# Kernel tuning notes

Hardware: AMD Instinct MI355X
Metric: run time of the kernel (lower is better)

Reference implementation:

```python
import jax, jax.numpy as jnp
import numpy as np

BITS = 4
MASK = (1 << BITS) - 1  # 15


def _dequant(qweight, scales, qzeros, groupsize):
    # qweight: [in//32*bits, out] int32; 8 nibbles packed per int32 along rows.
    out_f = qweight.shape[1]
    shifts = jnp.arange(0, 32, BITS, dtype=jnp.int32)  # [8]
    # [rows, 8, out] -> unpacked int weights in [0, 15]
    w = (qweight[:, None, :] >> shifts[None, :, None]) & MASK
    w = w.reshape(-1, groupsize, out_f)  # [n_groups, groupsize, out]
    s = scales.reshape(-1, 1, out_f)     # [n_groups, 1, out]
    z = qzeros.reshape(-1, 1, out_f)
    W = s * w.astype(scales.dtype) - z * s
    return W.reshape(-1, out_f)          # [in, out]


def setup_inputs() -> dict:
    key = jax.random.key(0)
    k1, k2, k3, k4, k5 = jax.random.split(key, 5)
    B, S, IN, OUT, G = 4, 2048, 4096, 4096, 64
    x = jax.random.normal(k1, (B, S, IN), dtype=jnp.float16)
    qweight = jax.random.randint(k2, (IN // 32 * BITS, OUT), 0, 2147483647, dtype=jnp.int32)
    scales = (jax.random.uniform(k3, (IN // G, OUT), dtype=jnp.float32) * 0.01 + 0.001).astype(jnp.float16)
    qzeros = (jax.random.uniform(k4, (IN // G, OUT), dtype=jnp.float32) * 15.0).astype(jnp.float16)
    bias = jax.random.normal(k5, (OUT,), dtype=jnp.float16)
    return {"x": x, "qweight": qweight, "scales": scales, "qzeros": qzeros,
            "bias": bias, "groupsize": G, "bits": BITS}


def reference(x, qweight, scales, qzeros, bias, groupsize, bits):
    W = _dequant(qweight, scales, qzeros, groupsize)  # [in, out] fp16
    return jnp.matmul(x, W) + bias
```

## Files before the change

kernel.cpp:

```cpp
#include <hip/hip_runtime.h>
#include <stdint.h>
#include <stddef.h>

typedef __bf16 bf16;
typedef __bf16 bf16x8 __attribute__((ext_vector_type(8)));
typedef float  f32x4  __attribute__((ext_vector_type(4)));

#define GLOBAL_AS(p) ((const __attribute__((address_space(1))) void*)(p))
#define LDS_AS(p)    ((__attribute__((address_space(3))) void*)(p))

__device__ __forceinline__ void gload_lds16(const bf16* g, bf16* l) {
    __builtin_amdgcn_global_load_lds(GLOBAL_AS(g), LDS_AS(l), 16, 0, 0);
}

__global__ __launch_bounds__(256)
void convert_x_kernel(const float* __restrict__ x, bf16* __restrict__ xb, long n8) {
    long t = (long)blockIdx.x * blockDim.x + threadIdx.x;
    if (t >= n8) return;
    const f32x4* p = (const f32x4*)(x + t * 8);
    f32x4 a = p[0], b = p[1];
    bf16x8 v;
#pragma unroll
    for (int j = 0; j < 4; ++j) { v[j] = (bf16)a[j]; v[4 + j] = (bf16)b[j]; }
    *(bf16x8*)(xb + t * 8) = v;
}

__global__ __launch_bounds__(256)
void dequant_wt64_kernel(const uint32_t* __restrict__ qw,
                         const float* __restrict__ scales,
                         const float* __restrict__ qzeros,
                         bf16* __restrict__ Wt,
                         int N, int K, int rows_per_group) {
    const int i = blockIdx.x * 256 + threadIdx.x;
    const int w = i >> 6, l = i & 63;
    const int nr8 = K >> 6;
    const int r8 = w % nr8;
    const int o  = (w / nr8) * 8 + (l >> 3);
    const int rr = l & 7;
    const int r  = r8 * 8 + rr;
    if (o >= N) return;
    const uint32_t q = qw[(size_t)r * N + o];
    const int g = r / rows_per_group;
    const float s = scales[(size_t)g * N + o];
    const float z = qzeros[(size_t)g * N + o];
    const float nsz = -s * z;
    bf16x8 v;
#pragma unroll
    for (int j = 0; j < 8; ++j)
        v[j] = (bf16)fmaf((float)((q >> (4 * j)) & 15u), s, nsz);
    *(bf16x8*)(Wt + ((size_t)r8 * N + o) * 64 + rr * 8) = v;
}

constexpr int BM2 = 256, BN2 = 256, BK2 = 64;

#define SB()    __builtin_amdgcn_sched_barrier(0)
#define BAR()   __builtin_amdgcn_s_barrier()
#define LGKM0() asm volatile("s_waitcnt lgkmcnt(0)" ::: "memory")
#define VMCNT(N) asm volatile("s_waitcnt vmcnt(" #N ")" ::: "memory")

#define PHASE_TAIL(A, B, IBASE)                          \
    SB();                                                \
    __builtin_amdgcn_s_setprio(1);                       \
    MFMA_HALF(A, B, IBASE);                              \
    __builtin_amdgcn_s_setprio(0);                       \
    SB();                                                \
    LGKM0();                                             \
    BAR();                                               \
    SB()

#define MFMA_HALF(A, B, IBASE)                                             \
    _Pragma("unroll")                                                      \
    for (int i_ = 0; i_ < 4; ++i_) {                                       \
        _Pragma("unroll")                                                  \
        for (int j_ = 0; j_ < 4; ++j_)                                     \
            acc[(IBASE) + i_][j_] = __builtin_amdgcn_mfma_f32_16x16x32_bf16( \
                (A)[(IBASE) + i_], (B)[j_], acc[(IBASE) + i_][j_], 0, 0, 0); \
    }

#define READ_A4(DST, BUF, KH, LO)                                          \
    _Pragma("unroll")                                                      \
    for (int i_ = (LO); i_ < (LO) + 4; ++i_)                               \
        DST[i_] = *(const bf16x8*)(&As[BUF][(wm * 128 + i_ * 16 + lrow) * 64 \
                                           + (((lhi + 4 * (KH)) ^ swz) * 8)]);
#define READ_B4(DST, BUF, KH)                                              \
    _Pragma("unroll")                                                      \
    for (int j_ = 0; j_ < 4; ++j_)                                         \
        DST[j_] = *(const bf16x8*)(&Bs[BUF][(wn * 64 + j_ * 16 + lrow) * 64 \
                                           + (((lhi + 4 * (KH)) ^ swz) * 8)]);

__global__ __launch_bounds__(512, 2)
void gemm8_kernel(const bf16* __restrict__ Ab,
                  const bf16* __restrict__ Bt,
                  const float* __restrict__ bias,
                  float* __restrict__ out,
                  int M, int N, int K, int nbx) {
    __shared__ __align__(16) bf16 As[2][BM2 * BK2];
    __shared__ __align__(16) bf16 Bs[2][BN2 * BK2];

    const int tid  = threadIdx.x;
    const int lane = tid & 63;
    const int wave = tid >> 6;
    const int wm = wave >> 2;
    const int wn = wave & 3;

    const int nwg = gridDim.x;
    int wg = blockIdx.x;
    {
        const int q = nwg >> 3, r = nwg & 7;
        const int xcd = wg & 7, off = wg >> 3;
        wg = (xcd < r ? xcd * (q + 1) : r * (q + 1) + (xcd - r) * q) + off;
    }
    const int nby = nwg / nbx;
    const int bx = wg / nby;
    const int by = wg % nby;
    const int m0 = by * BM2;
    const int n0 = bx * BN2;

    const int lrow = lane & 15;
    const int lhi  = lane >> 4;
    const int swz  = (lrow >> 1) & 7;

    const int NT = K >> 6;
    const int NI = NT >> 1;

    auto stageA = [&](int tIdx, int half, int buf) {
#pragma unroll
        for (int it = 0; it < 2; ++it) {
            const int q  = tid + it * 512;
            const int rl = q >> 3;
            const int cl = (q & 7) ^ ((rl >> 1) & 7);
            gload_lds16(Ab + (size_t)(m0 + half * 128 + rl) * K + tIdx * 64 + cl * 8,
                        &As[buf][half * 8192 + q * 8]);
        }
    };
    auto stageB = [&](int tIdx, int half, int buf) {
#pragma unroll
        for (int it = 0; it < 2; ++it) {
            const int q  = tid + it * 512;
            const int rl = q >> 3;
            const int cl = (q & 7) ^ ((rl >> 1) & 7);
            gload_lds16(Bt + ((size_t)tIdx * N + n0 + half * 128 + rl) * 64 + cl * 8,
                        &Bs[buf][half * 8192 + q * 8]);
        }
    };

    f32x4 acc[8][4];
#pragma unroll
    for (int i = 0; i < 8; ++i)
#pragma unroll
        for (int j = 0; j < 4; ++j) acc[i][j] = (f32x4){0.f, 0.f, 0.f, 0.f};

    stageA(0, 0, 0); stageA(0, 1, 0); stageB(0, 0, 0); stageB(0, 1, 0);
    stageA(1, 0, 1); stageA(1, 1, 1);
    VMCNT(4);
    BAR();
    SB();

    bf16x8 fa0[8], fa1[8], fb0[4], fb1[4];
    READ_A4(fa0, 0, 0, 0);
    READ_B4(fb0, 0, 0);
    LGKM0();
    SB();

    for (int i2 = 0; i2 < NI; ++i2) {
        const int t0  = 2 * i2;
        const int tB1 = t0 + 1;
        const int tS2 = (t0 + 2 < NT) ? t0 + 2 : NT - 1;
        const int tS3 = (t0 + 3 < NT) ? t0 + 3 : NT - 1;

        READ_A4(fa0, 0, 0, 4);
        stageB(tB1, 0, 1);
        stageB(tB1, 1, 1);
        PHASE_TAIL(fa0, fb0, 0);

        READ_A4(fa1, 0, 1, 0);
        READ_B4(fb1, 0, 1);
        PHASE_TAIL(fa0, fb0, 4);

        READ_A4(fa1, 0, 1, 4);
        stageB(tS2, 0, 0);
        stageB(tS2, 1, 0);
        PHASE_TAIL(fa1, fb1, 0);

        stageA(tS2, 0, 0);
        VMCNT(6);
        BAR();
        SB();
        READ_A4(fa0, 1, 0, 0);
        READ_B4(fb0, 1, 0);
        PHASE_TAIL(fa1, fb1, 4);

        READ_A4(fa0, 1, 0, 4);
        stageA(tS2, 1, 0);
        PHASE_TAIL(fa0, fb0, 0);

        READ_A4(fa1, 1, 1, 0);
        READ_B4(fb1, 1, 1);
        PHASE_TAIL(fa0, fb0, 4);

        READ_A4(fa1, 1, 1, 4);
        PHASE_TAIL(fa1, fb1, 0);

        stageA(tS3, 0, 1);
        stageA(tS3, 1, 1);
        VMCNT(4);
        BAR();
        SB();
        READ_A4(fa0, 0, 0, 0);
        READ_B4(fb0, 0, 0);
        PHASE_TAIL(fa1, fb1, 4);
    }

    asm volatile("s_waitcnt vmcnt(0)" ::: "memory");

#pragma unroll
    for (int j = 0; j < 4; ++j) {
        const int col = n0 + wn * 64 + j * 16 + lrow;
        const float bv = bias[col];
#pragma unroll
        for (int i = 0; i < 8; ++i) {
            const int rbase = m0 + wm * 128 + i * 16 + lhi * 4;
#pragma unroll
            for (int r = 0; r < 4; ++r)
                out[(size_t)(rbase + r) * N + col] = acc[i][j][r] + bv;
        }
    }
}

constexpr int BM = 128, BN = 128, BK = 32;

__global__ __launch_bounds__(256)
void gemm_fused_kernel(const float* __restrict__ Af,
                       const uint32_t* __restrict__ qw,
                       const float* __restrict__ scales,
                       const float* __restrict__ qzeros,
                       const float* __restrict__ bias,
                       float* __restrict__ out,
                       int M, int N, int K, int G) {
    __shared__ __align__(16) bf16 As2[BM * BK];
    __shared__ __align__(16) bf16 Bs2[BN * BK];

    const int tid  = threadIdx.x;
    const int lane = tid & 63;
    const int wave = tid >> 6;
    const int wmm = wave & 1;
    const int wnn = wave >> 1;
    const int m0 = blockIdx.y * BM;
    const int n0 = blockIdx.x * BN;

    const int lr = lane & 15;
    const int lk8 = (lane >> 4) * 8;

    f32x4 acc[4][4];
#pragma unroll
    for (int i = 0; i < 4; ++i)
#pragma unroll
        for (int j = 0; j < 4; ++j) acc[i][j] = (f32x4){0.f, 0.f, 0.f, 0.f};

    for (int kt = 0; kt < K; kt += BK) {
#pragma unroll
        for (int it = 0; it < 2; ++it) {
            const int c = tid + it * 256;
            const int row = c >> 2;
            const int kc  = (c & 3) * 8;
            const f32x4* p = (const f32x4*)(Af + (size_t)(m0 + row) * K + kt + kc);
            f32x4 a = p[0], b = p[1];
            bf16x8 v;
#pragma unroll
            for (int j = 0; j < 4; ++j) { v[j] = (bf16)a[j]; v[4 + j] = (bf16)b[j]; }
            *(bf16x8*)(As2 + row * BK + kc) = v;
        }
        const int g = kt / G;
#pragma unroll
        for (int it = 0; it < 2; ++it) {
            const int idx = tid + it * 256;
            const int rl = idx >> 7;
            const int nl = idx & 127;
            uint32_t q = qw[(size_t)(kt / 8 + rl) * N + n0 + nl];
            float s = scales[(size_t)g * N + n0 + nl];
            float z = qzeros[(size_t)g * N + n0 + nl];
            float nsz = -s * z;
            bf16x8 v;
#pragma unroll
            for (int j = 0; j < 8; ++j)
                v[j] = (bf16)fmaf((float)((q >> (4 * j)) & 15u), s, nsz);
            *(bf16x8*)(Bs2 + nl * BK + rl * 8) = v;
        }
        __syncthreads();

        bf16x8 a[4], b[4];
#pragma unroll
        for (int i = 0; i < 4; ++i)
            a[i] = *(const bf16x8*)(As2 + (wmm * 64 + i * 16 + lr) * BK + lk8);
#pragma unroll
        for (int j = 0; j < 4; ++j)
            b[j] = *(const bf16x8*)(Bs2 + (wnn * 64 + j * 16 + lr) * BK + lk8);

#pragma unroll
        for (int i = 0; i < 4; ++i)
#pragma unroll
            for (int j = 0; j < 4; ++j)
                acc[i][j] = __builtin_amdgcn_mfma_f32_16x16x32_bf16(
                    a[i], b[j], acc[i][j], 0, 0, 0);
        __syncthreads();
    }

#pragma unroll
    for (int j = 0; j < 4; ++j) {
        const int col = n0 + wnn * 64 + j * 16 + (lane & 15);
        const float bv = bias[col];
#pragma unroll
        for (int i = 0; i < 4; ++i) {
            const int rbase = m0 + wmm * 64 + i * 16 + (lane >> 4) * 4;
#pragma unroll
            for (int r = 0; r < 4; ++r)
                out[(size_t)(rbase + r) * N + col] = acc[i][j][r] + bv;
        }
    }
}

extern "C" void kernel_launch(void* const* d_in, const int* in_sizes, int n_in,
                              void* d_out, int out_size, void* d_ws, size_t ws_size,
                              hipStream_t stream) {
    const float*    x      = (const float*)d_in[0];
    const uint32_t* qw     = (const uint32_t*)d_in[1];
    const float*    scales = (const float*)d_in[2];
    const float*    qzeros = (const float*)d_in[3];
    const float*    bias   = (const float*)d_in[4];
    float*          out    = (float*)d_out;

    const int N = in_sizes[4];
    const int K = (in_sizes[1] / N) * 8;
    const int M = in_sizes[0] / K;
    const int G = K / (in_sizes[2] / N);

    const size_t xb_bytes = (size_t)M * K * sizeof(bf16);
    const size_t wt_bytes = (size_t)N * K * sizeof(bf16);

    const bool shape_ok = (M % BM2 == 0) && (N % BN2 == 0) && (K % 128 == 0) &&
                          (G % 8 == 0);

    if (shape_ok && ws_size >= xb_bytes + wt_bytes) {
        bf16* Xb = (bf16*)d_ws;
        bf16* Wt = (bf16*)((char*)d_ws + xb_bytes);
        const long n8 = (long)M * K / 8;
        convert_x_kernel<<<(int)((n8 + 255) / 256), 256, 0, stream>>>(x, Xb, n8);
        const long dq_threads = ((long)K >> 6) * (N / 8) * 64;
        dequant_wt64_kernel<<<(int)((dq_threads + 255) / 256), 256, 0, stream>>>(
            qw, scales, qzeros, Wt, N, K, G / 8);
        const int nbx = N / BN2;
        const int nwg = nbx * (M / BM2);
        gemm8_kernel<<<nwg, 512, 0, stream>>>(Xb, Wt, bias, out, M, N, K, nbx);
    } else {
        dim3 grid(N / BN, M / BM);
        gemm_fused_kernel<<<grid, 256, 0, stream>>>(
            x, qw, scales, qzeros, bias, out, M, N, K, G);
    }
}
```

Measured before the change: 500.0 us.

## Reschedule GEMM main loop with precomputed load pointers and merged barrier phases

After: 518.2 us. +3.6%, slower.

```diff
diff --git a/kernel.cpp b/kernel.cpp
--- a/kernel.cpp
+++ b/kernel.cpp
@@ -58,16 +58,6 @@
 #define LGKM0() asm volatile("s_waitcnt lgkmcnt(0)" ::: "memory")
 #define VMCNT(N) asm volatile("s_waitcnt vmcnt(" #N ")" ::: "memory")
 
-#define PHASE_TAIL(A, B, IBASE)                          \
-    SB();                                                \
-    __builtin_amdgcn_s_setprio(1);                       \
-    MFMA_HALF(A, B, IBASE);                              \
-    __builtin_amdgcn_s_setprio(0);                       \
-    SB();                                                \
-    LGKM0();                                             \
-    BAR();                                               \
-    SB()
-
 #define MFMA_HALF(A, B, IBASE)                                             \
     _Pragma("unroll")                                                      \
     for (int i_ = 0; i_ < 4; ++i_) {                                       \
@@ -76,6 +66,25 @@
             acc[(IBASE) + i_][j_] = __builtin_amdgcn_mfma_f32_16x16x32_bf16( \
                 (A)[(IBASE) + i_], (B)[j_], acc[(IBASE) + i_][j_], 0, 0, 0); \
     }
+
+#define PHASE_TAIL(A, B, IBASE)                          \
+    SB();                                                \
+    __builtin_amdgcn_s_setprio(1);                       \
+    MFMA_HALF(A, B, IBASE);                              \
+    __builtin_amdgcn_s_setprio(0);                       \
+    LGKM0();                                             \
+    BAR();                                               \
+    SB()
+
+#define PHASE_TAIL_VM4(A, B, IBASE)                      \
+    SB();                                                \
+    __builtin_amdgcn_s_setprio(1);                       \
+    MFMA_HALF(A, B, IBASE);                              \
+    __builtin_amdgcn_s_setprio(0);                       \
+    LGKM0();                                             \
+    VMCNT(4);                                            \
+    BAR();                                               \
+    SB()
 
 #define READ_A4(DST, BUF, KH, LO)                                          \
     _Pragma("unroll")                                                      \
@@ -123,25 +132,40 @@
     const int NT = K >> 6;
     const int NI = NT >> 1;
 
-    auto stageA = [&](int tIdx, int half, int buf) {
+    const bf16* aSrc[2][2];
+    const bf16* bSrc[2][2];
+#pragma unroll
+    for (int h = 0; h < 2; ++h)
 #pragma unroll
         for (int it = 0; it < 2; ++it) {
             const int q  = tid + it * 512;
             const int rl = q >> 3;
             const int cl = (q & 7) ^ ((rl >> 1) & 7);
-            gload_lds16(Ab + (size_t)(m0 + half * 128 + rl) * K + tIdx * 64 + cl * 8,
-                        &As[buf][half * 8192 + q * 8]);
-        }
+            aSrc[h][it] = Ab + (size_t)(m0 + h * 128 + rl) * K + cl * 8;
+            bSrc[h][it] = Bt + (size_t)(n0 + h * 128 + rl) * 64 + cl * 8;
+        }
+    const size_t aStride = 64;
+    const size_t bStride = (size_t)N * 64;
+
+    auto stageA = [&](int tIdx, int buf) {
+#pragma unroll
+        for (int h = 0; h < 2; ++h)
+#pragma unroll
+            for (int it = 0; it < 2; ++it) {
+                const int q = tid + it * 512;
+                gload_lds16(aSrc[h][it] + (size_t)tIdx * aStride,
+                            &As[buf][h * 8192 + q * 8]);
+            }
     };
-    auto stageB = [&](int tIdx, int half, int buf) {
-#pragma unroll
-        for (int it = 0; it < 2; ++it) {
-            const int q  = tid + it * 512;
-            const int rl = q >> 3;
-            const int cl = (q & 7) ^ ((rl >> 1) & 7);
-            gload_lds16(Bt + ((size_t)tIdx * N + n0 + half * 128 + rl) * 64 + cl * 8,
-                        &Bs[buf][half * 8192 + q * 8]);
-        }
+    auto stageB = [&](int tIdx, int buf) {
+#pragma unroll
+        for (int h = 0; h < 2; ++h)
+#pragma unroll
+            for (int it = 0; it < 2; ++it) {
+                const int q = tid + it * 512;
+                gload_lds16(bSrc[h][it] + (size_t)tIdx * bStride,
+                            &Bs[buf][h * 8192 + q * 8]);
+            }
     };
 
     f32x4 acc[8][4];
@@ -150,8 +174,7 @@
 #pragma unroll
         for (int j = 0; j < 4; ++j) acc[i][j] = (f32x4){0.f, 0.f, 0.f, 0.f};
 
-    stageA(0, 0, 0); stageA(0, 1, 0); stageB(0, 0, 0); stageB(0, 1, 0);
-    stageA(1, 0, 1); stageA(1, 1, 1);
+    stageA(0, 0); stageB(0, 0); stageA(1, 1);
     VMCNT(4);
     BAR();
     SB();
@@ -159,8 +182,6 @@
     bf16x8 fa0[8], fa1[8], fb0[4], fb1[4];
     READ_A4(fa0, 0, 0, 0);
     READ_B4(fb0, 0, 0);
-    LGKM0();
-    SB();
 
     for (int i2 = 0; i2 < NI; ++i2) {
         const int t0  = 2 * i2;
@@ -169,43 +190,33 @@
         const int tS3 = (t0 + 3 < NT) ? t0 + 3 : NT - 1;
 
         READ_A4(fa0, 0, 0, 4);
-        stageB(tB1, 0, 1);
-        stageB(tB1, 1, 1);
+        READ_B4(fb1, 0, 1);
+        stageB(tB1, 1);
         PHASE_TAIL(fa0, fb0, 0);
 
         READ_A4(fa1, 0, 1, 0);
-        READ_B4(fb1, 0, 1);
         PHASE_TAIL(fa0, fb0, 4);
 
         READ_A4(fa1, 0, 1, 4);
-        stageB(tS2, 0, 0);
-        stageB(tS2, 1, 0);
-        PHASE_TAIL(fa1, fb1, 0);
-
-        stageA(tS2, 0, 0);
-        VMCNT(6);
-        BAR();
-        SB();
+        stageB(tS2, 0);
+        PHASE_TAIL_VM4(fa1, fb1, 0);
+
         READ_A4(fa0, 1, 0, 0);
         READ_B4(fb0, 1, 0);
+        stageA(tS2, 0);
         PHASE_TAIL(fa1, fb1, 4);
 
         READ_A4(fa0, 1, 0, 4);
-        stageA(tS2, 1, 0);
+        READ_B4(fb1, 1, 1);
         PHASE_TAIL(fa0, fb0, 0);
 
         READ_A4(fa1, 1, 1, 0);
-        READ_B4(fb1, 1, 1);
+        READ_A4(fa1, 1, 1, 4);
         PHASE_TAIL(fa0, fb0, 4);
 
-        READ_A4(fa1, 1, 1, 4);
-        PHASE_TAIL(fa1, fb1, 0);
-
-        stageA(tS3, 0, 1);
-        stageA(tS3, 1, 1);
-        VMCNT(4);
-        BAR();
-        SB();
+        stageA(tS3, 1);
+        PHASE_TAIL_VM4(fa1, fb1, 0);
+
         READ_A4(fa0, 0, 0, 0);
         READ_B4(fb0, 0, 0);
         PHASE_TAIL(fa1, fb1, 4);
```
